# Performance work log

Hardware: AMD Instinct MI355X
Metric: run time of the kernel (lower is better)

## Reference

```python
import jax, jax.numpy as jnp
import numpy as np

B = 384
D_EMB = 256
NUM_TASKS = 4
MARGIN = 1.0
EPS = 1e-6  # F.pairwise_distance default eps, added to the difference


def setup_inputs() -> dict:
    key = jax.random.key(0)
    k1, k2 = jax.random.split(key)
    embeddings = jax.random.normal(k1, (B, D_EMB), dtype=jnp.float32)
    task_weights = jnp.ones((NUM_TASKS,), dtype=jnp.float32)
    task_rankings = jax.random.randint(k2, (B, NUM_TASKS), 0, 5, dtype=jnp.int32)
    return {"embeddings": embeddings, "task_weights": task_weights,
            "task_rankings": task_rankings}


def reference(embeddings, task_weights, task_rankings):
    # Pairwise euclidean distances, matching F.pairwise_distance: ||x - y + eps||_2
    diff = embeddings[:, None, :] - embeddings[None, :, :] + EPS      # [B, B, d]
    dist = jnp.sqrt(jnp.sum(diff * diff, axis=-1))                    # [B, B]

    # Triplet margin term for all (i, j, k): relu(D[i,j] - D[i,k] + margin)
    triple = jax.nn.relu(dist[:, :, None] - dist[:, None, :] + MARGIN)  # [B, B, B]

    total = jnp.zeros((), dtype=embeddings.dtype)
    for t in range(NUM_TASKS):  # small fixed loop over tasks
        r = task_rankings[:, t]
        gt = r[:, None] > r[None, :]                   # gt[a,b] = r[a] > r[b]
        mask = gt[:, :, None] & gt[None, :, :]         # (r_i>r_j) & (r_j>r_k)
        count = jnp.sum(mask).astype(embeddings.dtype)
        s = jnp.sum(jnp.where(mask, triple, jnp.zeros((), embeddings.dtype)))
        task_loss = s / jnp.maximum(count, 1.0)
        total = total + jnp.where(count > 0, task_weights[t] * task_loss, 0.0)
    return total
```

## Files before the change

### kernel.cpp

```cpp
#include <hip/hip_runtime.h>

#define NB   384
#define ND   256
#define EPSF 1e-6f
#define NBIN 512

#define WF_OFF   0
#define PART_OFF 16
#define ET_OFF   1024

__global__ __launch_bounds__(256) void prep_kernel(
    const float* __restrict__ emb,
    const float* __restrict__ tw,
    const int*   __restrict__ rank,
    float* __restrict__ ws)
{
    __shared__ float    t[32][33];
    __shared__ unsigned hist[20];

    const int tid = threadIdx.x;
    const int dt  = blockIdx.x & 7;
    const int jt  = blockIdx.x >> 3;
    const int c   = tid & 31;
    const int r8  = tid >> 5;

    #pragma unroll
    for (int p = 0; p < 4; ++p) {
        const int j = jt * 32 + r8 + p * 8;
        const int d = dt * 32 + c;
        t[r8 + p * 8][c] = emb[(size_t)j * ND + d];
    }
    __syncthreads();
    float* ET = ws + ET_OFF;
    #pragma unroll
    for (int p = 0; p < 4; ++p) {
        const int d = dt * 32 + r8 + p * 8;
        const int j = jt * 32 + c;
        ET[(size_t)d * NB + j] = t[c][r8 + p * 8] - EPSF;
    }

    if (blockIdx.x == 0) {
        if (tid < 20) hist[tid] = 0u;
        __syncthreads();
        for (int e = tid; e < NB * 4; e += 256)
            atomicAdd(&hist[(e & 3) * 5 + rank[e]], 1u);
        __syncthreads();
        if (tid < 4) {
            double cnt = 0.0;
            unsigned below = 0;
            #pragma unroll
            for (int v = 0; v < 5; ++v) {
                unsigned hv = hist[tid * 5 + v];
                unsigned above = (unsigned)NB - below - hv;
                cnt += (double)hv * (double)below * (double)above;
                below += hv;
            }
            ws[WF_OFF + tid] = (cnt > 0.0) ? (float)((double)tw[tid] / cnt) : 0.f;
        }
    }
}

__global__ __launch_bounds__(512) void loss_kernel(
    const float* __restrict__ emb,
    const float* __restrict__ et,
    const int*   __restrict__ rank,
    const float* __restrict__ wf,
    float* __restrict__ partial)
{
    __shared__ float    eil[ND];
    __shared__ unsigned hist[NBIN];
    __shared__ unsigned offs[NBIN + 1];
    __shared__ unsigned curs[NBIN];
    __shared__ unsigned srk[512];
    __shared__ unsigned long long cm[8][16];
    __shared__ unsigned cumtab[9][16];
    __shared__ unsigned wtot[8];
    __shared__ float    mmx[16];
    __shared__ float    sprm[2];
    __shared__ float    wfl[4];
    __shared__ float    red[8];

    const int p  = threadIdx.x;
    const int bi = blockIdx.x;
    const int wv = p >> 6;

    if (p < ND) eil[p] = emb[(size_t)bi * ND + p];
    if (p < 4)  wfl[p] = wf[p];
    hist[p] = 0u;
    if (p >= NB) srk[p] = 0xFFFFFFFFu;
    __syncthreads();

    float d = 0.f;
    if (p < NB) {
        float acc = 0.f;
        for (int d0 = 0; d0 < ND; d0 += 16) {
            float l[16];
            #pragma unroll
            for (int u = 0; u < 16; ++u)
                l[u] = et[(size_t)(d0 + u) * NB + p];
            #pragma unroll
            for (int u = 0; u < 16; ++u) {
                const float t = eil[d0 + u] - l[u];
                acc = fmaf(t, t, acc);
            }
        }
        d = sqrtf(acc);
    }

    float dl = (p < NB) ? d : 3.0e38f;
    float dh = (p < NB) ? d : -3.0e38f;
    #pragma unroll
    for (int off = 32; off > 0; off >>= 1) {
        dl = fminf(dl, __shfl_xor(dl, off, 64));
        dh = fmaxf(dh, __shfl_xor(dh, off, 64));
    }
    if ((p & 63) == 0) { mmx[wv] = dl; mmx[8 + wv] = dh; }
    __syncthreads();
    if (p == 0) {
        float mn = mmx[0], mx = mmx[8];
        #pragma unroll
        for (int w = 1; w < 8; ++w) {
            mn = fminf(mn, mmx[w]);
            mx = fmaxf(mx, mmx[8 + w]);
        }
        int S = (int)(511.0f / (mx - mn + 1.0f));
        if (S < 1) S = 1;
        sprm[0] = mn;
        sprm[1] = (float)S;
    }
    __syncthreads();
    const float dmin   = sprm[0];
    const float scaleF = sprm[1];
    const int   S      = (int)scaleF;

    int q = 0;
    unsigned rpk = 0xFFFFFFFFu;
    if (p < NB) {
        q = (int)((d - dmin) * scaleF);
        if (q > NBIN - 1) q = NBIN - 1;
        atomicAdd(&hist[q], 1u);
        const int4 r4 = *reinterpret_cast<const int4*>(rank + p * 4);
        rpk = (unsigned)r4.x | ((unsigned)r4.y << 8) |
              ((unsigned)r4.z << 16) | ((unsigned)r4.w << 24);
    }
    __syncthreads();

    const unsigned h = hist[p];
    unsigned inc = h;
    #pragma unroll
    for (int s = 1; s < 64; s <<= 1) {
        const unsigned o = __shfl_up(inc, s, 64);
        if ((p & 63) >= s) inc += o;
    }
    if ((p & 63) == 63) wtot[wv] = inc;
    __syncthreads();
    unsigned woff = 0;
    for (int w = 0; w < wv; ++w) woff += wtot[w];
    const unsigned excl = woff + inc - h;
    offs[p] = excl;
    curs[p] = excl;
    if (p == NBIN - 1) offs[NBIN] = excl + h;
    __syncthreads();

    if (p < NB) {
        const unsigned pos = atomicAdd(&curs[q], 1u);
        srk[pos] = rpk;
    }
    __syncthreads();

    const unsigned rsv = srk[p];
    #pragma unroll
    for (int t = 0; t < 4; ++t) {
        const unsigned rt = (rsv >> (8 * t)) & 0xFFu;
        #pragma unroll
        for (int w = 0; w < 4; ++w) {
            const unsigned long long m = __ballot(rt <= (unsigned)w);
            if ((p & 63) == 0) cm[wv][t * 4 + w] = m;
        }
    }
    __syncthreads();
    if (p < 16) {
        unsigned c = 0;
        #pragma unroll
        for (int w2 = 0; w2 < 8; ++w2) {
            cumtab[w2][p] = c;
            c += (unsigned)__popcll(cm[w2][p]);
        }
        cumtab[8][p] = c;
    }
    __syncthreads();

    float contrib = 0.f;
    if (p < NB) {
        const float thr = d + 1.0f;
        const int jidx = (q + S > NBIN) ? NBIN : (q + S);
        const int kidx = (q - S + 1 < 0) ? 0 : (q - S + 1);
        const unsigned P = offs[jidx];
        const unsigned L = offs[kidx];
        const int Pwv = (int)(P >> 6), Lwv = (int)(L >> 6);
        const unsigned long long Pmask = (1ull << (P & 63)) - 1ull;
        const unsigned long long Lmask = (1ull << (L & 63)) - 1ull;

        const int4 ri4 = *reinterpret_cast<const int4*>(rank + bi * 4);
        const unsigned rip = (unsigned)ri4.x | ((unsigned)ri4.y << 8) |
                             ((unsigned)ri4.z << 16) | ((unsigned)ri4.w << 24);

        float jacc = 0.f, kacc = 0.f;
        #pragma unroll
        for (int t = 0; t < 4; ++t) {
            const int ri = (int)((rip >> (8 * t)) & 0xFFu);
            const int ro = (int)((rpk >> (8 * t)) & 0xFFu);
            const float wt = wfl[t];
            if (ro > 0 && ro < ri) {
                const int w = t * 4 + (ro - 1);
                const unsigned N = cumtab[Pwv][w] +
                                   (unsigned)__popcll(cm[Pwv][w] & Pmask);
                jacc += wt * (float)N;
            }
            if (ro + 1 < ri) {
                const int wh = t * 4 + (ri - 1);
                const int wl = t * 4 + ro;
                const unsigned cLh = cumtab[Lwv][wh] +
                                     (unsigned)__popcll(cm[Lwv][wh] & Lmask);
                const unsigned cLl = cumtab[Lwv][wl] +
                                     (unsigned)__popcll(cm[Lwv][wl] & Lmask);
                const unsigned C = (cumtab[8][wh] - cLh) - (cumtab[8][wl] - cLl);
                kacc += wt * (float)C;
            }
        }
        contrib = jacc * thr - kacc * d;
    }

    #pragma unroll
    for (int off = 32; off > 0; off >>= 1)
        contrib += __shfl_down(contrib, off);
    if ((p & 63) == 0) red[wv] = contrib;
    __syncthreads();
    if (p == 0) {
        float s = 0.f;
        #pragma unroll
        for (int w = 0; w < 8; ++w) s += red[w];
        partial[bi] = s;
    }
}

__global__ __launch_bounds__(256) void reduce_kernel(
    const float* __restrict__ partial, float* __restrict__ out)
{
    __shared__ float r[4];
    const int tid = threadIdx.x;
    float t = 0.f;
    for (int p = tid; p < NB; p += 256) t += partial[p];
    #pragma unroll
    for (int off = 32; off > 0; off >>= 1)
        t += __shfl_down(t, off);
    if ((tid & 63) == 0) r[tid >> 6] = t;
    __syncthreads();
    if (tid == 0) out[0] = r[0] + r[1] + r[2] + r[3];
}

extern "C" void kernel_launch(void* const* d_in, const int* in_sizes, int n_in,
                              void* d_out, int out_size, void* d_ws, size_t ws_size,
                              hipStream_t stream)
{
    (void)in_sizes; (void)n_in; (void)out_size; (void)ws_size;
    const float* emb  = (const float*)d_in[0];
    const float* tw   = (const float*)d_in[1];
    const int*   rank = (const int*)d_in[2];
    float* ws  = (float*)d_ws;
    float* out = (float*)d_out;

    prep_kernel<<<96, 256, 0, stream>>>(emb, tw, rank, ws);
    loss_kernel<<<NB, 512, 0, stream>>>(emb, ws + ET_OFF, rank,
                                        ws + WF_OFF, ws + PART_OFF);
    reduce_kernel<<<1, 256, 0, stream>>>(ws + PART_OFF, out);
}
```

Baseline: 24.19 us.

## Compute distances via Gram matrix and fuse final reduction into loss kernel

Replaces the transpose-based prep kernel and per-block direct distance computation with a tiled Gram-matrix kernel. Distances come from ||a||^2+||b||^2-2ab, which drops the eps term and changes numerics. The loss kernel now uses 384 threads with no padding lanes. The separate reduce kernel is removed in favour of a last-block atomic ticket, at the cost of an extra memset launch and the precision risk of the Gram identity.

```diff
diff --git a/kernel.cpp b/kernel.cpp
--- a/kernel.cpp
+++ b/kernel.cpp
@@ -2,42 +2,63 @@
 
 #define NB   384
 #define ND   256
-#define EPSF 1e-6f
-#define NBIN 512
+#define NBIN 384
 
 #define WF_OFF   0
+#define TICK_OFF 8
 #define PART_OFF 16
-#define ET_OFF   1024
-
-__global__ __launch_bounds__(256) void prep_kernel(
+#define G_OFF    512
+
+__global__ __launch_bounds__(256) void gram_kernel(
     const float* __restrict__ emb,
     const float* __restrict__ tw,
     const int*   __restrict__ rank,
     float* __restrict__ ws)
 {
-    __shared__ float    t[32][33];
+    __shared__ float As[32][70];
+    __shared__ float Bs[32][70];
     __shared__ unsigned hist[20];
 
-    const int tid = threadIdx.x;
-    const int dt  = blockIdx.x & 7;
-    const int jt  = blockIdx.x >> 3;
-    const int c   = tid & 31;
-    const int r8  = tid >> 5;
-
-    #pragma unroll
-    for (int p = 0; p < 4; ++p) {
-        const int j = jt * 32 + r8 + p * 8;
-        const int d = dt * 32 + c;
-        t[r8 + p * 8][c] = emb[(size_t)j * ND + d];
-    }
-    __syncthreads();
-    float* ET = ws + ET_OFF;
-    #pragma unroll
-    for (int p = 0; p < 4; ++p) {
-        const int d = dt * 32 + r8 + p * 8;
-        const int j = jt * 32 + c;
-        ET[(size_t)d * NB + j] = t[c][r8 + p * 8] - EPSF;
-    }
+    const int tid  = threadIdx.x;
+    const int bi   = blockIdx.x % 12;
+    const int bj   = blockIdx.x / 12;
+    const int tx   = tid & 15, ty = tid >> 4;
+    const int srow = tid >> 3, scol = (tid & 7) * 8;
+
+    float a00 = 0.f, a01 = 0.f, a10 = 0.f, a11 = 0.f;
+    for (int kc = 0; kc < ND; kc += 64) {
+        const float2* pa = reinterpret_cast<const float2*>(
+            emb + (size_t)(bi * 32 + srow) * ND + kc + scol);
+        const float2* pb = reinterpret_cast<const float2*>(
+            emb + (size_t)(bj * 32 + srow) * ND + kc + scol);
+        float2 va0 = pa[0], va1 = pa[1], va2 = pa[2], va3 = pa[3];
+        float2 vb0 = pb[0], vb1 = pb[1], vb2 = pb[2], vb3 = pb[3];
+        *reinterpret_cast<float2*>(&As[srow][scol + 0]) = va0;
+        *reinterpret_cast<float2*>(&As[srow][scol + 2]) = va1;
+        *reinterpret_cast<float2*>(&As[srow][scol + 4]) = va2;
+        *reinterpret_cast<float2*>(&As[srow][scol + 6]) = va3;
+        *reinterpret_cast<float2*>(&Bs[srow][scol + 0]) = vb0;
+        *reinterpret_cast<float2*>(&Bs[srow][scol + 2]) = vb1;
+        *reinterpret_cast<float2*>(&Bs[srow][scol + 4]) = vb2;
+        *reinterpret_cast<float2*>(&Bs[srow][scol + 6]) = vb3;
+        __syncthreads();
+        #pragma unroll 8
+        for (int k = 0; k < 64; ++k) {
+            const float A0 = As[ty * 2][k],     A1 = As[ty * 2 + 1][k];
+            const float B0 = Bs[tx * 2][k],     B1 = Bs[tx * 2 + 1][k];
+            a00 = fmaf(A0, B0, a00);
+            a01 = fmaf(A0, B1, a01);
+            a10 = fmaf(A1, B0, a10);
+            a11 = fmaf(A1, B1, a11);
+        }
+        __syncthreads();
+    }
+    float* G = ws + G_OFF;
+    const int r = bi * 32 + ty * 2, c = bj * 32 + tx * 2;
+    float2 s0; s0.x = a00; s0.y = a01;
+    float2 s1; s1.x = a10; s1.y = a11;
+    *reinterpret_cast<float2*>(&G[(size_t)r * NB + c])       = s0;
+    *reinterpret_cast<float2*>(&G[(size_t)(r + 1) * NB + c]) = s1;
 
     if (blockIdx.x == 0) {
         if (tid < 20) hist[tid] = 0u;
@@ -60,70 +81,57 @@
     }
 }
 
-__global__ __launch_bounds__(512) void loss_kernel(
-    const float* __restrict__ emb,
-    const float* __restrict__ et,
+__global__ __launch_bounds__(NB) void loss_kernel(
+    const float* __restrict__ G,
     const int*   __restrict__ rank,
     const float* __restrict__ wf,
-    float* __restrict__ partial)
+    float*       __restrict__ partial,
+    unsigned*    __restrict__ tick,
+    float*       __restrict__ out)
 {
-    __shared__ float    eil[ND];
     __shared__ unsigned hist[NBIN];
     __shared__ unsigned offs[NBIN + 1];
     __shared__ unsigned curs[NBIN];
-    __shared__ unsigned srk[512];
-    __shared__ unsigned long long cm[8][16];
-    __shared__ unsigned cumtab[9][16];
-    __shared__ unsigned wtot[8];
-    __shared__ float    mmx[16];
+    __shared__ unsigned srk[NB];
+    __shared__ unsigned long long cm[7][16];
+    __shared__ unsigned cumtab[7][16];
+    __shared__ unsigned wtot[6];
+    __shared__ float    mmx[12];
     __shared__ float    sprm[2];
     __shared__ float    wfl[4];
-    __shared__ float    red[8];
+    __shared__ float    red[6];
+    __shared__ int      lastflag;
 
     const int p  = threadIdx.x;
     const int bi = blockIdx.x;
     const int wv = p >> 6;
 
-    if (p < ND) eil[p] = emb[(size_t)bi * ND + p];
     if (p < 4)  wfl[p] = wf[p];
+    if (p < 16) cm[6][p] = 0ull;
     hist[p] = 0u;
-    if (p >= NB) srk[p] = 0xFFFFFFFFu;
-    __syncthreads();
-
-    float d = 0.f;
-    if (p < NB) {
-        float acc = 0.f;
-        for (int d0 = 0; d0 < ND; d0 += 16) {
-            float l[16];
-            #pragma unroll
-            for (int u = 0; u < 16; ++u)
-                l[u] = et[(size_t)(d0 + u) * NB + p];
-            #pragma unroll
-            for (int u = 0; u < 16; ++u) {
-                const float t = eil[d0 + u] - l[u];
-                acc = fmaf(t, t, acc);
-            }
-        }
-        d = sqrtf(acc);
-    }
-
-    float dl = (p < NB) ? d : 3.0e38f;
-    float dh = (p < NB) ? d : -3.0e38f;
+
+    const float ni  = G[(size_t)bi * NB + bi];
+    const float g   = G[(size_t)bi * NB + p];
+    const float npp = G[(size_t)p * (NB + 1)];
+    const float d   = sqrtf(fmaxf(ni + npp - 2.f * g, 0.f));
+
+    float dl = (p == bi) ? 3.0e38f : d;
+    float dh = d;
     #pragma unroll
     for (int off = 32; off > 0; off >>= 1) {
         dl = fminf(dl, __shfl_xor(dl, off, 64));
         dh = fmaxf(dh, __shfl_xor(dh, off, 64));
     }
-    if ((p & 63) == 0) { mmx[wv] = dl; mmx[8 + wv] = dh; }
+    if ((p & 63) == 0) { mmx[wv] = dl; mmx[6 + wv] = dh; }
     __syncthreads();
     if (p == 0) {
-        float mn = mmx[0], mx = mmx[8];
-        #pragma unroll
-        for (int w = 1; w < 8; ++w) {
+        float mn = mmx[0], mx = mmx[6];
+        #pragma unroll
+        for (int w = 1; w < 6; ++w) {
             mn = fminf(mn, mmx[w]);
-            mx = fmaxf(mx, mmx[8 + w]);
-        }
-        int S = (int)(511.0f / (mx - mn + 1.0f));
+            mx = fmaxf(mx, mmx[6 + w]);
+        }
+        int S = (int)(383.0f / (mx - mn + 1.0f));
         if (S < 1) S = 1;
         sprm[0] = mn;
         sprm[1] = (float)S;
@@ -133,16 +141,13 @@
     const float scaleF = sprm[1];
     const int   S      = (int)scaleF;
 
-    int q = 0;
-    unsigned rpk = 0xFFFFFFFFu;
-    if (p < NB) {
-        q = (int)((d - dmin) * scaleF);
-        if (q > NBIN - 1) q = NBIN - 1;
-        atomicAdd(&hist[q], 1u);
-        const int4 r4 = *reinterpret_cast<const int4*>(rank + p * 4);
-        rpk = (unsigned)r4.x | ((unsigned)r4.y << 8) |
-              ((unsigned)r4.z << 16) | ((unsigned)r4.w << 24);
-    }
+    int q = (int)((d - dmin) * scaleF);
+    if (q < 0) q = 0;
+    if (q > NBIN - 1) q = NBIN - 1;
+    atomicAdd(&hist[q], 1u);
+    const int4 r4 = *reinterpret_cast<const int4*>(rank + p * 4);
+    const unsigned rpk = (unsigned)r4.x | ((unsigned)r4.y << 8) |
+                         ((unsigned)r4.z << 16) | ((unsigned)r4.w << 24);
     __syncthreads();
 
     const unsigned h = hist[p];
@@ -162,10 +167,8 @@
     if (p == NBIN - 1) offs[NBIN] = excl + h;
     __syncthreads();
 
-    if (p < NB) {
-        const unsigned pos = atomicAdd(&curs[q], 1u);
-        srk[pos] = rpk;
-    }
+    const unsigned pos = atomicAdd(&curs[q], 1u);
+    srk[pos] = rpk;
     __syncthreads();
 
     const unsigned rsv = srk[p];
@@ -182,54 +185,51 @@
     if (p < 16) {
         unsigned c = 0;
         #pragma unroll
-        for (int w2 = 0; w2 < 8; ++w2) {
+        for (int w2 = 0; w2 < 6; ++w2) {
             cumtab[w2][p] = c;
             c += (unsigned)__popcll(cm[w2][p]);
         }
-        cumtab[8][p] = c;
-    }
-    __syncthreads();
-
-    float contrib = 0.f;
-    if (p < NB) {
-        const float thr = d + 1.0f;
-        const int jidx = (q + S > NBIN) ? NBIN : (q + S);
-        const int kidx = (q - S + 1 < 0) ? 0 : (q - S + 1);
-        const unsigned P = offs[jidx];
-        const unsigned L = offs[kidx];
-        const int Pwv = (int)(P >> 6), Lwv = (int)(L >> 6);
-        const unsigned long long Pmask = (1ull << (P & 63)) - 1ull;
-        const unsigned long long Lmask = (1ull << (L & 63)) - 1ull;
-
-        const int4 ri4 = *reinterpret_cast<const int4*>(rank + bi * 4);
-        const unsigned rip = (unsigned)ri4.x | ((unsigned)ri4.y << 8) |
-                             ((unsigned)ri4.z << 16) | ((unsigned)ri4.w << 24);
-
-        float jacc = 0.f, kacc = 0.f;
-        #pragma unroll
-        for (int t = 0; t < 4; ++t) {
-            const int ri = (int)((rip >> (8 * t)) & 0xFFu);
-            const int ro = (int)((rpk >> (8 * t)) & 0xFFu);
-            const float wt = wfl[t];
-            if (ro > 0 && ro < ri) {
-                const int w = t * 4 + (ro - 1);
-                const unsigned N = cumtab[Pwv][w] +
-                                   (unsigned)__popcll(cm[Pwv][w] & Pmask);
-                jacc += wt * (float)N;
-            }
-            if (ro + 1 < ri) {
-                const int wh = t * 4 + (ri - 1);
-                const int wl = t * 4 + ro;
-                const unsigned cLh = cumtab[Lwv][wh] +
-                                     (unsigned)__popcll(cm[Lwv][wh] & Lmask);
-                const unsigned cLl = cumtab[Lwv][wl] +
-                                     (unsigned)__popcll(cm[Lwv][wl] & Lmask);
-                const unsigned C = (cumtab[8][wh] - cLh) - (cumtab[8][wl] - cLl);
-                kacc += wt * (float)C;
-            }
-        }
-        contrib = jacc * thr - kacc * d;
-    }
+        cumtab[6][p] = c;
+    }
+    __syncthreads();
+
+    const float thr = d + 1.0f;
+    const int jidx = (q + S > NBIN) ? NBIN : (q + S);
+    const int kidx = (q - S + 1 < 0) ? 0 : (q - S + 1);
+    const unsigned P = offs[jidx];
+    const unsigned L = offs[kidx];
+    const int Pwv = (int)(P >> 6), Lwv = (int)(L >> 6);
+    const unsigned long long Pmask = (1ull << (P & 63)) - 1ull;
+    const unsigned long long Lmask = (1ull << (L & 63)) - 1ull;
+
+    const int4 ri4 = *reinterpret_cast<const int4*>(rank + bi * 4);
+    const unsigned rip = (unsigned)ri4.x | ((unsigned)ri4.y << 8) |
+                         ((unsigned)ri4.z << 16) | ((unsigned)ri4.w << 24);
+
+    float jacc = 0.f, kacc = 0.f;
+    #pragma unroll
+    for (int t = 0; t < 4; ++t) {
+        const int ri = (int)((rip >> (8 * t)) & 0xFFu);
+        const int ro = (int)((rpk >> (8 * t)) & 0xFFu);
+        const float wt = wfl[t];
+        if (ro > 0 && ro < ri) {
+            const int w = t * 4 + (ro - 1);
+            const unsigned N = cumtab[Pwv][w] +
+                               (unsigned)__popcll(cm[Pwv][w] & Pmask);
+            jacc += wt * (float)N;
+        }
+        if (ro + 1 < ri) {
+            const int wh = t * 4 + (ri - 1);
+            const int wl = t * 4 + ro;
+            const unsigned cLh = cumtab[Lwv][wh] +
+                                 (unsigned)__popcll(cm[Lwv][wh] & Lmask);
+            const unsigned cLl = cumtab[Lwv][wl] +
+                                 (unsigned)__popcll(cm[Lwv][wl] & Lmask);
+            const unsigned C = (cumtab[6][wh] - cLh) - (cumtab[6][wl] - cLl);
+            kacc += wt * (float)C;
+        }
+    }
+    float contrib = jacc * thr - kacc * d;
 
     #pragma unroll
     for (int off = 32; off > 0; off >>= 1)
@@ -239,24 +239,31 @@
     if (p == 0) {
         float s = 0.f;
         #pragma unroll
-        for (int w = 0; w < 8; ++w) s += red[w];
-        partial[bi] = s;
-    }
-}
-
-__global__ __launch_bounds__(256) void reduce_kernel(
-    const float* __restrict__ partial, float* __restrict__ out)
-{
-    __shared__ float r[4];
-    const int tid = threadIdx.x;
-    float t = 0.f;
-    for (int p = tid; p < NB; p += 256) t += partial[p];
-    #pragma unroll
-    for (int off = 32; off > 0; off >>= 1)
-        t += __shfl_down(t, off);
-    if ((tid & 63) == 0) r[tid >> 6] = t;
-    __syncthreads();
-    if (tid == 0) out[0] = r[0] + r[1] + r[2] + r[3];
+        for (int w = 0; w < 6; ++w) s += red[w];
+        __hip_atomic_store(&partial[bi], s, __ATOMIC_RELEASE,
+                           __HIP_MEMORY_SCOPE_AGENT);
+        const unsigned t = __hip_atomic_fetch_add(tick, 1u, __ATOMIC_ACQ_REL,
+                                                  __HIP_MEMORY_SCOPE_AGENT);
+        lastflag = (t == NB - 1) ? 1 : 0;
+    }
+    __syncthreads();
+
+    if (lastflag) {
+        __threadfence();
+        float v = __hip_atomic_load(&partial[p], __ATOMIC_RELAXED,
+                                    __HIP_MEMORY_SCOPE_AGENT);
+        #pragma unroll
+        for (int off = 32; off > 0; off >>= 1)
+            v += __shfl_down(v, off);
+        if ((p & 63) == 0) red[wv] = v;
+        __syncthreads();
+        if (p == 0) {
+            float s = 0.f;
+            #pragma unroll
+            for (int w = 0; w < 6; ++w) s += red[w];
+            out[0] = s;
+        }
+    }
 }
 
 extern "C" void kernel_launch(void* const* d_in, const int* in_sizes, int n_in,
@@ -270,8 +277,10 @@
     float* ws  = (float*)d_ws;
     float* out = (float*)d_out;
 
-    prep_kernel<<<96, 256, 0, stream>>>(emb, tw, rank, ws);
-    loss_kernel<<<NB, 512, 0, stream>>>(emb, ws + ET_OFF, rank,
-                                        ws + WF_OFF, ws + PART_OFF);
-    reduce_kernel<<<1, 256, 0, stream>>>(ws + PART_OFF, out);
+    hipMemsetAsync(ws + TICK_OFF, 0, sizeof(unsigned), stream);
+    gram_kernel<<<144, 256, 0, stream>>>(emb, tw, rank, ws);
+    loss_kernel<<<NB, NB, 0, stream>>>(ws + G_OFF, rank, ws + WF_OFF,
+                                       ws + PART_OFF,
+                                       reinterpret_cast<unsigned*>(ws + TICK_OFF),
+                                       out);
 }
```

Measured after the change: 32.88 us. 1.36x slower.
